# Performance work log

Hardware: AMD Instinct MI355X
Metric: run time of the kernel (lower is better)

## Reference

```python
import jax, jax.numpy as jnp
import numpy as np

NEG_SLOPE = 0.01  # torch F.leaky_relu default
BN_EPS = 1e-5
N_GRAPHS = 256


def _bn(x, gamma, beta):
    # training-mode BatchNorm1d per head over the node axis; x: [N, H, O]
    mu = x.mean(axis=0)
    var = x.var(axis=0)
    return (x - mu) * jax.lax.rsqrt(var + BN_EPS) * gamma + beta


def _gat_layer(h, src, dst, snorm, fcW, aS, aD, gamma, beta):
    # h: [N, Din]; fcW: [H, Din, O]; aS/aD/gamma/beta: [H, O]
    N = h.shape[0]
    z = jnp.einsum('nd,hdo->nho', h, fcW)                 # [N, H, O]
    el = jnp.einsum('nho,ho->nh', z, aS)                  # attn_fc src half
    er = jnp.einsum('nho,ho->nh', z, aD)                  # attn_fc dst half
    e = jax.nn.leaky_relu(el[src] + er[dst], NEG_SLOPE)   # [E, H]
    emax = jax.ops.segment_max(e, dst, num_segments=N)    # softmax over in-edges
    ee = jnp.exp(e - emax[dst])
    denom = jax.ops.segment_sum(ee, dst, num_segments=N)
    alpha = ee / denom[dst]                               # [E, H]
    msg = alpha[:, :, None] * z[src]                      # [E, H, O]
    agg = jax.ops.segment_sum(msg, dst, num_segments=N)   # [N, H, O]
    agg = agg * snorm[:, None, None]                      # graph_norm
    agg = _bn(agg, gamma, beta)                           # batch_norm
    out = jax.nn.elu(agg).reshape(N, -1)                  # concat heads
    return h + out                                        # residual (Din == H*O)


def setup_inputs() -> dict:
    key = jax.random.key(0)
    ks = jax.random.split(key, 32)
    N, E, G = 50000, 1600000, N_GRAPHS
    DIN, H, O, D, NC = 128, 8, 16, 128, 10
    L_mid = 3  # L-1 multi-head layers

    graph_ids = jnp.sort(jax.random.randint(ks[0], (N,), 0, G))
    counts = jax.ops.segment_sum(jnp.ones((N,), jnp.float32), graph_ids, num_segments=G)
    snorm = (1.0 / jnp.sqrt(jnp.maximum(counts, 1.0)))[graph_ids]  # nodes_num_norm_sqrt
    src = jax.random.randint(ks[1], (E,), 0, N)
    dst = jax.random.randint(ks[2], (E,), 0, N)

    def nrm(k, shape, s=0.1):
        return jax.random.normal(k, shape, jnp.float32) * s

    return {
        'nodes_feat': jax.random.normal(ks[3], (N, DIN), jnp.float32),
        'snorm': snorm,
        'emb_W': nrm(ks[4], (DIN, D)), 'emb_b': jnp.zeros((D,), jnp.float32),
        'fcW': nrm(ks[5], (L_mid, H, D, O)),
        'aS': nrm(ks[6], (L_mid, H, O)), 'aD': nrm(ks[7], (L_mid, H, O)),
        'gamma': jnp.ones((L_mid, H, O), jnp.float32),
        'beta': jnp.zeros((L_mid, H, O), jnp.float32),
        'fcW_last': nrm(ks[8], (1, D, D)),
        'aS_last': nrm(ks[9], (1, D)), 'aD_last': nrm(ks[10], (1, D)),
        'g_last': jnp.ones((1, D), jnp.float32), 'b_last': jnp.zeros((1, D), jnp.float32),
        'w1': nrm(ks[11], (D, D // 2)), 'b1': jnp.zeros((D // 2,), jnp.float32),
        'w2': nrm(ks[12], (D // 2, D // 4)), 'b2': jnp.zeros((D // 4,), jnp.float32),
        'w3': nrm(ks[13], (D // 4, NC)), 'b3': jnp.zeros((NC,), jnp.float32),
        'src': src, 'dst': dst, 'graph_ids': graph_ids,
    }


def reference(nodes_feat, snorm, emb_W, emb_b, fcW, aS, aD, gamma, beta,
              fcW_last, aS_last, aD_last, g_last, b_last,
              w1, b1, w2, b2, w3, b3, src, dst, graph_ids):
    h = nodes_feat @ emb_W + emb_b                        # embedding_h
    for l in range(fcW.shape[0]):                         # L-1 multi-head GAT layers
        h = _gat_layer(h, src, dst, snorm, fcW[l], aS[l], aD[l], gamma[l], beta[l])
    h = _gat_layer(h, src, dst, snorm, fcW_last, aS_last, aD_last, g_last, b_last)
    # mean_nodes readout over variable-size graphs
    counts = jax.ops.segment_sum(jnp.ones_like(snorm), graph_ids, num_segments=N_GRAPHS)
    hg = jax.ops.segment_sum(h, graph_ids, num_segments=N_GRAPHS)
    hg = hg / jnp.maximum(counts, 1.0)[:, None]           # [G, D]
    # MLPReadout: D -> D/2 -> D/4 -> n_classes
    y = jax.nn.relu(hg @ w1 + b1)
    y = jax.nn.relu(y @ w2 + b2)
    return y @ w3 + b3
```

## Files before the change

### kernel.cpp

```cpp
#include <hip/hip_runtime.h>
#include <hip/hip_bf16.h>
#include <hip/hip_fp16.h>

typedef __hip_bfloat16 bf16;
typedef __attribute__((ext_vector_type(8))) short short8;
typedef __attribute__((ext_vector_type(4))) float floatx4;

__device__ __forceinline__ float ldc(const void* p, size_t i, int code) {
    if (code == 1) return __bfloat162float(((const bf16*)p)[i]);
    if (code == 2) return __half2float(((const __half*)p)[i]);
    return ((const float*)p)[i];
}
__device__ __forceinline__ void stc(void* p, size_t i, int code, float v) {
    if (code == 1) ((bf16*)p)[i] = __float2bfloat16(v);
    else if (code == 2) ((__half*)p)[i] = __float2half(v);
    else ((float*)p)[i] = v;
}
__device__ __forceinline__ unsigned int pk2(float a, float b) {
    unsigned int ua = __float_as_uint(a); ua += 0x7fffu + ((ua >> 16) & 1u);
    unsigned int ub = __float_as_uint(b); ub += 0x7fffu + ((ub >> 16) & 1u);
    return (ua >> 16) | (ub & 0xffff0000u);
}

__global__ void k_detect(const unsigned short* __restrict__ g, int* __restrict__ code) {
    unsigned short a = g[0], b = g[1], c = g[2], d = g[3];
    int r;
    if (a == 0x3F80 && b == 0x3F80 && c == 0x3F80 && d == 0x3F80) r = 1;
    else if (a == 0x3C00 && b == 0x3C00 && c == 0x3C00 && d == 0x3C00) r = 2;
    else r = 3;
    *code = r;
}

__global__ void k_zero_i(int* p, int n) { int i = blockIdx.x * 256 + threadIdx.x; if (i < n) p[i] = 0; }
__global__ void k_zero_f(float* p, int n) { int i = blockIdx.x * 256 + threadIdx.x; if (i < n) p[i] = 0.f; }
__global__ void k_cvt(float* __restrict__ dst, const void* __restrict__ src, int n,
                      const int* __restrict__ codep) {
    int code = *codep;
    int i = blockIdx.x * 256 + threadIdx.x;
    if (i < n) dst[i] = ldc(src, i, code);
}
__global__ void k_sent(void* o, int n, float v, const int* codep) {
    int code = *codep;
    int i = blockIdx.x * 256 + threadIdx.x;
    if (i < n) stc(o, i, code, v);
}

struct CvtArgs { const void* src[16]; int off[17]; };
__global__ void k_cvt_all(float* __restrict__ dst, CvtArgs a,
                          const int* __restrict__ codep, int total) {
    int i = blockIdx.x * 256 + threadIdx.x;
    if (i >= total) return;
    int code = *codep;
    int seg = 0;
    #pragma unroll
    for (int k = 0; k < 15; ++k) seg += (i >= a.off[k + 1]) ? 1 : 0;
    dst[i] = ldc(a.src[seg], i - a.off[seg], code);
}

#define ETILE 8192
__global__ __launch_bounds__(256) void k_bcount(const int* __restrict__ dst,
        int* __restrict__ bcnt, int E, int nbuck) {
    __shared__ int h[200];
    int t = threadIdx.x;
    for (int i = t; i < nbuck; i += 256) h[i] = 0;
    __syncthreads();
    int e0 = blockIdx.x * ETILE;
    int n = min(ETILE, E - e0);
    for (int i = t; i < n; i += 256) atomicAdd(&h[dst[e0 + i] >> 8], 1);
    __syncthreads();
    for (int i = t; i < nbuck; i += 256)
        if (h[i]) atomicAdd(&bcnt[i], h[i]);
}

__global__ void k_scan(const int* __restrict__ cnt, int* __restrict__ off,
                       int* __restrict__ cur, int n) {
    __shared__ int sums[1024];
    int tid = threadIdx.x;
    int C = (n + 1023) >> 10;
    int lo = tid * C, hi = min(lo + C, n);
    int s = 0;
    for (int i = lo; i < hi; ++i) s += cnt[i];
    sums[tid] = s;
    __syncthreads();
    for (int o = 1; o < 1024; o <<= 1) {
        int v = (tid >= o) ? sums[tid - o] : 0;
        __syncthreads();
        sums[tid] += v;
        __syncthreads();
    }
    int run = (tid > 0) ? sums[tid - 1] : 0;
    for (int i = lo; i < hi; ++i) { off[i] = run; cur[i] = run; run += cnt[i]; }
    if (tid == 1023) off[n] = sums[1023];
}

__global__ __launch_bounds__(256) void k_bscat(const int* __restrict__ src,
        const int* __restrict__ dst, int* __restrict__ bcur,
        unsigned int* __restrict__ ebuf, int E, int nbuck) {
    __shared__ unsigned int eord[ETILE];
    __shared__ int cnt[200], lst[200], cur[200], gb[200];
    int t = threadIdx.x;
    int e0 = blockIdx.x * ETILE;
    int n = min(ETILE, E - e0);
    for (int i = t; i < nbuck; i += 256) cnt[i] = 0;
    __syncthreads();
    for (int i = t; i < n; i += 256) atomicAdd(&cnt[dst[e0 + i] >> 8], 1);
    __syncthreads();
    if (t == 0) {
        int run = 0;
        for (int b = 0; b < nbuck; ++b) { int c = cnt[b]; lst[b] = run; cur[b] = run; run += c; }
    }
    __syncthreads();
    for (int b = t; b < nbuck; b += 256)
        gb[b] = cnt[b] ? atomicAdd(&bcur[b], cnt[b]) : 0;
    for (int i = t; i < n; i += 256) {
        int d = dst[e0 + i];
        int pos = atomicAdd(&cur[d >> 8], 1);
        eord[pos] = ((unsigned int)d << 16) | (unsigned int)src[e0 + i];
    }
    __syncthreads();
    for (int i = t; i < n; i += 256) {
        unsigned int pk = eord[i];
        int b = pk >> 24;
        ebuf[gb[b] + (i - lst[b])] = pk;
    }
}

__global__ __launch_bounds__(256) void k_fscatter(const unsigned int* __restrict__ ebuf,
        const int* __restrict__ boff, int* __restrict__ row_off,
        unsigned short* __restrict__ col_src, int N, int E) {
    __shared__ int cnt[256], cur[256];
    int b = blockIdx.x, t = threadIdx.x;
    int lo = boff[b], hi = boff[b + 1];
    int nodelo = b << 8;
    cnt[t] = 0;
    __syncthreads();
    for (int j = lo + t; j < hi; j += 256)
        atomicAdd(&cnt[(int)(ebuf[j] >> 16) - nodelo], 1);
    __syncthreads();
    if (t == 0) {
        int run = lo;
        for (int i = 0; i < 256; ++i) { int c = cnt[i]; cur[i] = run; cnt[i] = run; run += c; }
    }
    __syncthreads();
    int node = nodelo + t;
    if (node < N) row_off[node] = cnt[t];
    if (t == 0 && b == (int)gridDim.x - 1) row_off[N] = E;
    for (int j = lo + t; j < hi; j += 256) {
        unsigned int pk = ebuf[j];
        int pos = atomicAdd(&cur[(int)(pk >> 16) - nodelo], 1);
        col_src[pos] = (unsigned short)(pk & 0xffffu);
    }
}

#define WB_STRIDE 136
#define WB_MAT 19584
__global__ void k_wtrans(const void* __restrict__ fcW, const void* __restrict__ fcW_last,
                         const void* __restrict__ emb_W,
                         const float* __restrict__ aSf, const float* __restrict__ aDf,
                         const float* __restrict__ aSlf, const float* __restrict__ aDlf,
                         unsigned short* __restrict__ Wb, const int* __restrict__ codep) {
    int code = *codep;
    int idx = blockIdx.x * 256 + threadIdx.x;
    if (idx >= 5 * WB_MAT) return;
    int m = idx / WB_MAT, rem = idx % WB_MAT;
    int c = rem / WB_STRIDE, k = rem % WB_STRIDE;
    float v = 0.f;
    if (k < 128) {
        if (m == 0) {
            if (c < 128) v = ldc(emb_W, k * 128 + c, code);
        } else if (m <= 3) {
            int l = m - 1;
            if (c < 128) v = ldc(fcW, l * 16384 + (c >> 4) * 2048 + k * 16 + (c & 15), code);
            else if (c < 136) {
                int hh = c - 128; float s = 0.f;
                for (int o = 0; o < 16; ++o)
                    s += ldc(fcW, l * 16384 + hh * 2048 + k * 16 + o, code) * aSf[l * 128 + hh * 16 + o];
                v = s;
            } else {
                int hh = c - 136; float s = 0.f;
                for (int o = 0; o < 16; ++o)
                    s += ldc(fcW, l * 16384 + hh * 2048 + k * 16 + o, code) * aDf[l * 128 + hh * 16 + o];
                v = s;
            }
        } else {
            if (c < 128) v = ldc(fcW_last, k * 128 + c, code);
            else if (c == 128) { float s = 0.f; for (int o = 0; o < 128; ++o) s += ldc(fcW_last, k * 128 + o, code) * aSlf[o]; v = s; }
            else if (c == 129) { float s = 0.f; for (int o = 0; o < 128; ++o) s += ldc(fcW_last, k * 128 + o, code) * aDlf[o]; v = s; }
        }
    }
    Wb[idx] = (unsigned short)(pk2(v, 0.f) & 0xffffu);
}

__global__ __launch_bounds__(256) void k_gemm(const void* __restrict__ Av, int a_raw,
        const int* __restrict__ codep, const unsigned short* __restrict__ Wbm,
        const float* __restrict__ bias, float* __restrict__ outf,
        unsigned int* __restrict__ zb,
        float* __restrict__ el, float* __restrict__ er, int H, int N) {
    __shared__ unsigned short Wl[WB_MAT];
    int tid = threadIdx.x;
    {
        const uint4* s4 = (const uint4*)Wbm;
        uint4* d4 = (uint4*)Wl;
        for (int i = tid; i < WB_MAT / 8; i += 256) d4[i] = s4[i];
    }
    int wave = tid >> 6, lane = tid & 63;
    int c15 = lane & 15, quad = lane >> 4;
    int rowb = blockIdx.x * 64 + wave * 16;
    int myrow = rowb + c15;
    bool rowok = myrow < N;
    int code = a_raw ? *codep : 3;

    floatx4 acc[9];
    #pragma unroll
    for (int i = 0; i < 9; ++i) acc[i] = (floatx4){0.f, 0.f, 0.f, 0.f};

    __syncthreads();
    #pragma unroll
    for (int ks = 0; ks < 4; ++ks) {
        int k0 = ks * 32 + quad * 8;
        short8 a;
        if (!rowok) {
            a = (short8){0, 0, 0, 0, 0, 0, 0, 0};
        } else if (code == 1) {
            union { uint4 u; short8 s; } cv;
            cv.u = *(const uint4*)((const unsigned short*)Av + (size_t)myrow * 128 + k0);
            a = cv.s;
        } else if (code == 3) {
            const float* ap = (const float*)Av + (size_t)myrow * 128 + k0;
            float4 x = *(const float4*)ap;
            float4 y = *(const float4*)(ap + 4);
            union { uint4 u; short8 s; } cv;
            cv.u = make_uint4(pk2(x.x, x.y), pk2(x.z, x.w), pk2(y.x, y.y), pk2(y.z, y.w));
            a = cv.s;
        } else {
            const __half* ap = (const __half*)Av + (size_t)myrow * 128 + k0;
            union { uint4 u; short8 s; } cv;
            cv.u = make_uint4(pk2(__half2float(ap[0]), __half2float(ap[1])),
                              pk2(__half2float(ap[2]), __half2float(ap[3])),
                              pk2(__half2float(ap[4]), __half2float(ap[5])),
                              pk2(__half2float(ap[6]), __half2float(ap[7])));
            a = cv.s;
        }
        #pragma unroll
        for (int ct = 0; ct < 9; ++ct) {
            union { uint4 u; short8 s; } bv;
            bv.u = *(const uint4*)&Wl[(ct * 16 + c15) * WB_STRIDE + k0];
            acc[ct] = __builtin_amdgcn_mfma_f32_16x16x32_bf16(a, bv.s, acc[ct], 0, 0, 0);
        }
    }

    if (zb == nullptr) {
        #pragma unroll
        for (int ct = 0; ct < 8; ++ct) {
            int c = ct * 16 + c15;
            float bj = bias ? bias[c] : 0.f;
            #pragma unroll
            for (int r = 0; r < 4; ++r) {
                int n = rowb + quad * 4 + r;
                if (n < N) outf[(size_t)n * 128 + c] = acc[ct][r] + bj;
            }
        }
    } else {
        #pragma unroll
        for (int ct = 0; ct < 8; ++ct) {
            #pragma unroll
            for (int r = 0; r < 4; ++r) {
                float v = acc[ct][r];
                float vx = __shfl_xor(v, 1);
                if ((c15 & 1) == 0) {
                    int n = rowb + quad * 4 + r;
                    if (n < N) zb[(size_t)n * 64 + ct * 8 + (c15 >> 1)] = pk2(v, vx);
                }
            }
        }
        #pragma unroll
        for (int r = 0; r < 4; ++r) {
            int n = rowb + quad * 4 + r;
            if (n < N) {
                float v = acc[8][r];
                if (c15 < H) el[n * H + c15] = v;
                else if (c15 < 2 * H) er[n * H + (c15 - H)] = v;
            }
        }
    }
}

__global__ __launch_bounds__(256) void k_agg(const unsigned int* __restrict__ zb,
        const float* __restrict__ el, const float* __restrict__ er,
        const int* __restrict__ row_off, const unsigned short* __restrict__ col_src,
        const float* __restrict__ snormf, float* __restrict__ agg,
        int N, int H, int hshift) {
    int n = blockIdx.x * 4 + (threadIdx.x >> 6);
    if (n >= N) return;
    int lane = threadIdx.x & 63;
    int hh = lane >> hshift;
    float ern = er[n * H + hh];
    int beg = row_off[n], end = row_off[n + 1];
    float l = 0.f, a0 = 0.f, a1 = 0.f;
    int j = beg;
    if (H == 8) {
        for (; j + 8 <= end; j += 8) {
            int sv = col_src[j + (lane & 7)];
            float e = el[sv * 8 + (lane >> 3)] + ern;
            e = (e > 0.f) ? e : 0.01f * e;
            float w = __expf(fminf(e, 60.f));
            #pragma unroll
            for (int i = 0; i < 8; ++i) {
                float wi = __shfl(w, i, 8);
                int si = col_src[j + i];
                unsigned int v = zb[(size_t)si * 64 + lane];
                l += wi;
                a0 = fmaf(wi, __uint_as_float(v << 16), a0);
                a1 = fmaf(wi, __uint_as_float(v & 0xffff0000u), a1);
            }
        }
    } else {
        for (; j + 16 <= end; j += 16) {
            int sv = col_src[j + (lane & 15)];
            float e = el[sv] + ern;
            e = (e > 0.f) ? e : 0.01f * e;
            float w = __expf(fminf(e, 60.f));
            #pragma unroll
            for (int i = 0; i < 16; ++i) {
                float wi = __shfl(w, i, 16);
                int si = col_src[j + i];
                unsigned int v = zb[(size_t)si * 64 + lane];
                l += wi;
                a0 = fmaf(wi, __uint_as_float(v << 16), a0);
                a1 = fmaf(wi, __uint_as_float(v & 0xffff0000u), a1);
            }
        }
    }
    for (; j < end; ++j) {
        int sa = col_src[j];
        float ea = el[sa * H + hh] + ern;
        unsigned int va = zb[(size_t)sa * 64 + lane];
        ea = (ea > 0.f) ? ea : 0.01f * ea;
        float wa = __expf(fminf(ea, 60.f));
        l += wa;
        a0 = fmaf(wa, __uint_as_float(va << 16), a0);
        a1 = fmaf(wa, __uint_as_float(va & 0xffff0000u), a1);
    }
    float sn = snormf[n];
    float inv = (end > beg) ? sn / l : 0.f;
    *(float2*)&agg[(size_t)n * 128 + 2 * lane] = make_float2(a0 * inv, a1 * inv);
}

#define BN_BLOCKS 256
__global__ void k_bnstats1(const float* __restrict__ agg, float* __restrict__ pstats, int N) {
    int c = threadIdx.x;
    float s = 0.f, q = 0.f;
    for (int n = blockIdx.x; n < N; n += gridDim.x) {
        float v = agg[(size_t)n * 128 + c];
        s += v; q += v * v;
    }
    pstats[blockIdx.x * 256 + c] = s;
    pstats[blockIdx.x * 256 + 128 + c] = q;
}
__global__ void k_bnstats2(const float* __restrict__ pstats, float* __restrict__ stats, int nb) {
    int c = threadIdx.x;
    float s0 = 0.f, s1 = 0.f, s2 = 0.f, s3 = 0.f;
    int b = 0;
    for (; b + 3 < nb; b += 4) {
        s0 += pstats[b * 256 + c];
        s1 += pstats[(b + 1) * 256 + c];
        s2 += pstats[(b + 2) * 256 + c];
        s3 += pstats[(b + 3) * 256 + c];
    }
    for (; b < nb; ++b) s0 += pstats[b * 256 + c];
    stats[c] = (s0 + s1) + (s2 + s3);
}
__global__ void k_bnapply(const float* __restrict__ agg, const float* __restrict__ stats,
        const float* __restrict__ gamma, const float* __restrict__ beta,
        float* __restrict__ h, int N) {
    int idx = blockIdx.x * 256 + threadIdx.x;
    if (idx >= N * 128) return;
    int c = idx & 127;
    float invN = 1.0f / (float)N;
    float mu = stats[c] * invN;
    float var = fmaxf(stats[128 + c] * invN - mu * mu, 0.f);
    float x = agg[idx];
    float xn = (x - mu) * rsqrtf(var + 1e-5f) * gamma[c] + beta[c];
    float y = (xn > 0.f) ? xn : (__expf(xn) - 1.0f);
    h[idx] += y;
}

__global__ void k_gsum(const float* __restrict__ h, const int* __restrict__ gids,
                       float* __restrict__ hg, float* __restrict__ gcnt, int N) {
    int c = threadIdx.x;
    int base = blockIdx.x * 64;
    int endi = min(base + 64, N);
    int gprev = -1; float acc = 0.f; int cnt = 0;
    for (int n = base; n < endi; ++n) {
        int g = gids[n];
        if (g != gprev) {
            if (gprev >= 0) {
                atomicAdd(&hg[gprev * 128 + c], acc);
                if (c == 0) atomicAdd(&gcnt[gprev], (float)cnt);
            }
            gprev = g; acc = 0.f; cnt = 0;
        }
        acc += h[(size_t)n * 128 + c];
        ++cnt;
    }
    if (gprev >= 0) {
        atomicAdd(&hg[gprev * 128 + c], acc);
        if (c == 0) atomicAdd(&gcnt[gprev], (float)cnt);
    }
}
__global__ void k_mlp(const float* __restrict__ hg, const float* __restrict__ gcnt,
        const float* __restrict__ w1, const float* __restrict__ b1,
        const float* __restrict__ w2, const float* __restrict__ b2,
        const float* __restrict__ w3, const float* __restrict__ b3,
        void* __restrict__ out, const int* __restrict__ codep) {
    __shared__ float xs[128], y1[64], y2[32];
    int g = blockIdx.x, tid = threadIdx.x;
    float inv = 1.0f / fmaxf(gcnt[g], 1.0f);
    xs[tid]      = hg[g * 128 + tid] * inv;
    xs[tid + 64] = hg[g * 128 + 64 + tid] * inv;
    __syncthreads();
    float a = b1[tid];
    for (int k = 0; k < 128; ++k) a = fmaf(xs[k], w1[k * 64 + tid], a);
    y1[tid] = fmaxf(a, 0.f);
    __syncthreads();
    if (tid < 32) {
        float a2 = b2[tid];
        for (int k = 0; k < 64; ++k) a2 = fmaf(y1[k], w2[k * 32 + tid], a2);
        y2[tid] = fmaxf(a2, 0.f);
    }
    __syncthreads();
    if (tid < 10) {
        float a3 = b3[tid];
        for (int k = 0; k < 32; ++k) a3 = fmaf(y2[k], w3[k * 10 + tid], a3);
        stc(out, g * 10 + tid, *codep, a3);
    }
}

extern "C" void kernel_launch(void* const* d_in, const int* in_sizes, int n_in,
                              void* d_out, int out_size, void* d_ws, size_t ws_size,
                              hipStream_t stream) {
    const void* nodes_feat = d_in[0];
    const void* snorm      = d_in[1];
    const void* emb_W      = d_in[2];
    const void* fcW        = d_in[4];
    const void* gamma      = d_in[7];
    const void* fcW_last   = d_in[9];
    const int*  src        = (const int*)d_in[20];
    const int*  dst        = (const int*)d_in[21];
    const int*  gids       = (const int*)d_in[22];

    const int N = 50000, E = 1600000, G = 256;
    const int NBUCK = (N + 255) >> 8;
    const int NTILE = (E + ETILE - 1) / ETILE;

    char* p = (char*)d_ws;
    auto alloc = [&](size_t bytes) { char* r = p; p += (bytes + 255) & ~(size_t)255; return r; };
    int*   code    = (int*)alloc(256);
    float* h       = (float*)alloc((size_t)N * 128 * 4);
    unsigned int* zb = (unsigned int*)alloc((size_t)N * 64 * 4);
    float* agg     = (float*)alloc((size_t)N * 128 * 4);
    float* el      = (float*)alloc((size_t)N * 8 * 4);
    float* er      = (float*)alloc((size_t)N * 8 * 4);
    int*   bcnt    = (int*)alloc((size_t)NBUCK * 4);
    int*   boff    = (int*)alloc((size_t)(NBUCK + 1) * 4);
    int*   bcur    = (int*)alloc((size_t)NBUCK * 4);
    unsigned int* ebuf = (unsigned int*)alloc((size_t)E * 4);
    int*   row_off = (int*)alloc((size_t)(N + 1) * 4);
    unsigned short* col_src = (unsigned short*)alloc((size_t)E * 2);
    unsigned short* Wb = (unsigned short*)alloc((size_t)5 * WB_MAT * 2);
    float* pstats  = (float*)alloc((size_t)BN_BLOCKS * 256 * 4);
    float* stats   = (float*)alloc(256 * 4);
    float* hg      = (float*)alloc((size_t)G * 128 * 4 + (size_t)G * 4);
    float* gcnt    = hg + (size_t)G * 128;
    float* snormf  = (float*)alloc((size_t)N * 4);
    float* params  = (float*)alloc(29226 * 4);

    const int OFF[17] = {0, 16384, 16512, 16896, 17280, 17664, 18048, 18176,
                         18304, 18432, 18560, 26752, 26816, 28864, 28896, 29216, 29226};
    float* emb_bf = params + OFF[1];
    float* aSf    = params + OFF[2];
    float* aDf    = params + OFF[3];
    float* gf     = params + OFF[4];
    float* bf     = params + OFF[5];
    float* aSlf   = params + OFF[6];
    float* aDlf   = params + OFF[7];
    float* glf    = params + OFF[8];
    float* blf    = params + OFF[9];
    float* w1f    = params + OFF[10];
    float* b1f    = params + OFF[11];
    float* w2f    = params + OFF[12];
    float* b2f_   = params + OFF[13];
    float* w3f    = params + OFF[14];
    float* b3f    = params + OFF[15];

    k_detect<<<1, 1, 0, stream>>>((const unsigned short*)gamma, code);

    bool ok = (n_in == 23) && (out_size == G * 10) &&
              (in_sizes[0] == N * 128) && (in_sizes[1] == N) &&
              (in_sizes[4] == 3 * 8 * 128 * 16) && (in_sizes[7] == 384) &&
              (in_sizes[9] == 16384) &&
              (in_sizes[20] == E) && (in_sizes[21] == E) && (in_sizes[22] == N);
    size_t need = (size_t)(p - (char*)d_ws);
    if (!ok || ws_size < need) {
        k_sent<<<(out_size + 255) / 256, 256, 0, stream>>>(d_out, out_size, ok ? 123.0f : 150.0f, code);
        return;
    }

    CvtArgs ca;
    const int srcidx[16] = {2, 3, 5, 6, 7, 8, 10, 11, 12, 13, 14, 15, 16, 17, 18, 19};
    for (int k = 0; k < 16; ++k) ca.src[k] = d_in[srcidx[k]];
    for (int k = 0; k < 17; ++k) ca.off[k] = OFF[k];
    k_cvt_all<<<(29226 + 255) / 256, 256, 0, stream>>>(params, ca, code, 29226);
    k_cvt<<<(N + 255) / 256, 256, 0, stream>>>(snormf, snorm, N, code);
    k_wtrans<<<(5 * WB_MAT + 255) / 256, 256, 0, stream>>>(
        fcW, fcW_last, emb_W, aSf, aDf, aSlf, aDlf, Wb, code);

    k_zero_i<<<1, 256, 0, stream>>>(bcnt, NBUCK);
    k_bcount<<<NTILE, 256, 0, stream>>>(dst, bcnt, E, NBUCK);
    k_scan<<<1, 1024, 0, stream>>>(bcnt, boff, bcur, NBUCK);
    k_bscat<<<NTILE, 256, 0, stream>>>(src, dst, bcur, ebuf, E, NBUCK);
    k_fscatter<<<NBUCK, 256, 0, stream>>>(ebuf, boff, row_off, col_src, N, E);

    int gblk = (N + 63) / 64;
    k_gemm<<<gblk, 256, 0, stream>>>(nodes_feat, 1, code, Wb, emb_bf, h,
                                     nullptr, nullptr, nullptr, 0, N);

    for (int l = 0; l < 4; ++l) {
        const unsigned short* Wl_ = Wb + (size_t)(l + 1) * WB_MAT;
        const float *gl, *bl; int H, hshift;
        if (l < 3) { gl = gf + l * 128; bl = bf + l * 128; H = 8; hshift = 3; }
        else       { gl = glf;          bl = blf;          H = 1; hshift = 6; }
        k_gemm<<<gblk, 256, 0, stream>>>(h, 0, code, Wl_, nullptr, nullptr,
                                         zb, el, er, H, N);
        k_agg<<<(N + 3) / 4, 256, 0, stream>>>(zb, el, er, row_off, col_src, snormf,
                                               agg, N, H, hshift);
        k_bnstats1<<<BN_BLOCKS, 128, 0, stream>>>(agg, pstats, N);
        k_bnstats2<<<1, 256, 0, stream>>>(pstats, stats, BN_BLOCKS);
        k_bnapply<<<(N * 128 + 255) / 256, 256, 0, stream>>>(agg, stats, gl, bl, h, N);
    }

    k_zero_f<<<(G * 129 + 255) / 256, 256, 0, stream>>>(hg, G * 129);
    k_gsum<<<(N + 63) / 64, 128, 0, stream>>>(h, gids, hg, gcnt, N);
    k_mlp<<<G, 64, 0, stream>>>(hg, gcnt, w1f, b1f, w2f, b2f_, w3f, b3f, d_out, code);
}
```

Before: 928.7 us.

## Split each node's edges across wave halves with 8-byte gathers in GAT aggregation

Measured after the change: 921.3 us. Within noise of the previous version (-0.8%).

```diff
diff --git a/kernel.cpp b/kernel.cpp
--- a/kernel.cpp
+++ b/kernel.cpp
@@ -33,19 +33,13 @@
 
 __global__ void k_zero_i(int* p, int n) { int i = blockIdx.x * 256 + threadIdx.x; if (i < n) p[i] = 0; }
 __global__ void k_zero_f(float* p, int n) { int i = blockIdx.x * 256 + threadIdx.x; if (i < n) p[i] = 0.f; }
-__global__ void k_cvt(float* __restrict__ dst, const void* __restrict__ src, int n,
-                      const int* __restrict__ codep) {
-    int code = *codep;
-    int i = blockIdx.x * 256 + threadIdx.x;
-    if (i < n) dst[i] = ldc(src, i, code);
-}
 __global__ void k_sent(void* o, int n, float v, const int* codep) {
     int code = *codep;
     int i = blockIdx.x * 256 + threadIdx.x;
     if (i < n) stc(o, i, code, v);
 }
 
-struct CvtArgs { const void* src[16]; int off[17]; };
+struct CvtArgs { const void* src[17]; int off[18]; };
 __global__ void k_cvt_all(float* __restrict__ dst, CvtArgs a,
                           const int* __restrict__ codep, int total) {
     int i = blockIdx.x * 256 + threadIdx.x;
@@ -53,7 +47,7 @@
     int code = *codep;
     int seg = 0;
     #pragma unroll
-    for (int k = 0; k < 15; ++k) seg += (i >= a.off[k + 1]) ? 1 : 0;
+    for (int k = 0; k < 16; ++k) seg += (i >= a.off[k + 1]) ? 1 : 0;
     dst[i] = ldc(a.src[seg], i - a.off[seg], code);
 }
 
@@ -289,61 +283,82 @@
         const float* __restrict__ el, const float* __restrict__ er,
         const int* __restrict__ row_off, const unsigned short* __restrict__ col_src,
         const float* __restrict__ snormf, float* __restrict__ agg,
-        int N, int H, int hshift) {
+        int N, int H) {
     int n = blockIdx.x * 4 + (threadIdx.x >> 6);
     if (n >= N) return;
     int lane = threadIdx.x & 63;
-    int hh = lane >> hshift;
-    float ern = er[n * H + hh];
+    int half = lane >> 5;
+    int sub = lane & 31;
+    int hha = (H == 8) ? (sub >> 2) : 0;
+    float er_t = er[n * H + hha];
+    float er_w = (H == 8) ? er[n * 8 + (lane >> 3)] : er_t;
     int beg = row_off[n], end = row_off[n + 1];
-    float l = 0.f, a0 = 0.f, a1 = 0.f;
+    float l = 0.f, c0 = 0.f, c1 = 0.f, c2 = 0.f, c3 = 0.f;
     int j = beg;
     if (H == 8) {
         for (; j + 8 <= end; j += 8) {
             int sv = col_src[j + (lane & 7)];
-            float e = el[sv * 8 + (lane >> 3)] + ern;
+            float e = el[sv * 8 + (lane >> 3)] + er_w;
             e = (e > 0.f) ? e : 0.01f * e;
             float w = __expf(fminf(e, 60.f));
             #pragma unroll
-            for (int i = 0; i < 8; ++i) {
-                float wi = __shfl(w, i, 8);
+            for (int p = 0; p < 4; ++p) {
+                int i = 2 * p + half;
+                float wi = __shfl(w, (hha << 3) + i);
                 int si = col_src[j + i];
-                unsigned int v = zb[(size_t)si * 64 + lane];
+                uint2 v = *(const uint2*)(zb + (size_t)si * 64 + sub * 2);
                 l += wi;
-                a0 = fmaf(wi, __uint_as_float(v << 16), a0);
-                a1 = fmaf(wi, __uint_as_float(v & 0xffff0000u), a1);
+                c0 = fmaf(wi, __uint_as_float(v.x << 16), c0);
+                c1 = fmaf(wi, __uint_as_float(v.x & 0xffff0000u), c1);
+                c2 = fmaf(wi, __uint_as_float(v.y << 16), c2);
+                c3 = fmaf(wi, __uint_as_float(v.y & 0xffff0000u), c3);
             }
         }
     } else {
         for (; j + 16 <= end; j += 16) {
             int sv = col_src[j + (lane & 15)];
-            float e = el[sv] + ern;
+            float e = el[sv] + er_w;
             e = (e > 0.f) ? e : 0.01f * e;
             float w = __expf(fminf(e, 60.f));
             #pragma unroll
-            for (int i = 0; i < 16; ++i) {
+            for (int p = 0; p < 8; ++p) {
+                int i = 2 * p + half;
                 float wi = __shfl(w, i, 16);
                 int si = col_src[j + i];
-                unsigned int v = zb[(size_t)si * 64 + lane];
+                uint2 v = *(const uint2*)(zb + (size_t)si * 64 + sub * 2);
                 l += wi;
-                a0 = fmaf(wi, __uint_as_float(v << 16), a0);
-                a1 = fmaf(wi, __uint_as_float(v & 0xffff0000u), a1);
-            }
-        }
-    }
-    for (; j < end; ++j) {
-        int sa = col_src[j];
-        float ea = el[sa * H + hh] + ern;
-        unsigned int va = zb[(size_t)sa * 64 + lane];
-        ea = (ea > 0.f) ? ea : 0.01f * ea;
-        float wa = __expf(fminf(ea, 60.f));
-        l += wa;
-        a0 = fmaf(wa, __uint_as_float(va << 16), a0);
-        a1 = fmaf(wa, __uint_as_float(va & 0xffff0000u), a1);
-    }
-    float sn = snormf[n];
-    float inv = (end > beg) ? sn / l : 0.f;
-    *(float2*)&agg[(size_t)n * 128 + 2 * lane] = make_float2(a0 * inv, a1 * inv);
+                c0 = fmaf(wi, __uint_as_float(v.x << 16), c0);
+                c1 = fmaf(wi, __uint_as_float(v.x & 0xffff0000u), c1);
+                c2 = fmaf(wi, __uint_as_float(v.y << 16), c2);
+                c3 = fmaf(wi, __uint_as_float(v.y & 0xffff0000u), c3);
+            }
+        }
+    }
+    for (; j < end; j += 2) {
+        int idx = j + half;
+        bool act = idx < end;
+        int si = col_src[act ? idx : j];
+        float e = el[si * H + hha] + er_t;
+        e = (e > 0.f) ? e : 0.01f * e;
+        float w = act ? __expf(fminf(e, 60.f)) : 0.f;
+        uint2 v = *(const uint2*)(zb + (size_t)si * 64 + sub * 2);
+        l += w;
+        c0 = fmaf(w, __uint_as_float(v.x << 16), c0);
+        c1 = fmaf(w, __uint_as_float(v.x & 0xffff0000u), c1);
+        c2 = fmaf(w, __uint_as_float(v.y << 16), c2);
+        c3 = fmaf(w, __uint_as_float(v.y & 0xffff0000u), c3);
+    }
+    l  += __shfl_xor(l, 32);
+    c0 += __shfl_xor(c0, 32);
+    c1 += __shfl_xor(c1, 32);
+    c2 += __shfl_xor(c2, 32);
+    c3 += __shfl_xor(c3, 32);
+    if (half == 0) {
+        float sn = snormf[n];
+        float inv = (end > beg) ? sn / l : 0.f;
+        float4 o = make_float4(c0 * inv, c1 * inv, c2 * inv, c3 * inv);
+        *(float4*)&agg[(size_t)n * 128 + 4 * sub] = o;
+    }
 }
 
 #define BN_BLOCKS 256
@@ -452,6 +467,7 @@
     const int N = 50000, E = 1600000, G = 256;
     const int NBUCK = (N + 255) >> 8;
     const int NTILE = (E + ETILE - 1) / ETILE;
+    const int PTOT = 29226 + N;
 
     char* p = (char*)d_ws;
     auto alloc = [&](size_t bytes) { char* r = p; p += (bytes + 255) & ~(size_t)255; return r; };
@@ -472,11 +488,10 @@
     float* stats   = (float*)alloc(256 * 4);
     float* hg      = (float*)alloc((size_t)G * 128 * 4 + (size_t)G * 4);
     float* gcnt    = hg + (size_t)G * 128;
-    float* snormf  = (float*)alloc((size_t)N * 4);
-    float* params  = (float*)alloc(29226 * 4);
-
-    const int OFF[17] = {0, 16384, 16512, 16896, 17280, 17664, 18048, 18176,
-                         18304, 18432, 18560, 26752, 26816, 28864, 28896, 29216, 29226};
+    float* params  = (float*)alloc((size_t)PTOT * 4);
+
+    const int OFF[18] = {0, 16384, 16512, 16896, 17280, 17664, 18048, 18176,
+                         18304, 18432, 18560, 26752, 26816, 28864, 28896, 29216, 29226, PTOT};
     float* emb_bf = params + OFF[1];
     float* aSf    = params + OFF[2];
     float* aDf    = params + OFF[3];
@@ -492,6 +507,7 @@
     float* b2f_   = params + OFF[13];
     float* w3f    = params + OFF[14];
     float* b3f    = params + OFF[15];
+    float* snormf = params + OFF[16];
 
     k_detect<<<1, 1, 0, stream>>>((const unsigned short*)gamma, code);
 
@@ -507,11 +523,10 @@
     }
 
     CvtArgs ca;
-    const int srcidx[16] = {2, 3, 5, 6, 7, 8, 10, 11, 12, 13, 14, 15, 16, 17, 18, 19};
-    for (int k = 0; k < 16; ++k) ca.src[k] = d_in[srcidx[k]];
-    for (int k = 0; k < 17; ++k) ca.off[k] = OFF[k];
-    k_cvt_all<<<(29226 + 255) / 256, 256, 0, stream>>>(params, ca, code, 29226);
-    k_cvt<<<(N + 255) / 256, 256, 0, stream>>>(snormf, snorm, N, code);
+    const int srcidx[17] = {2, 3, 5, 6, 7, 8, 10, 11, 12, 13, 14, 15, 16, 17, 18, 19, 1};
+    for (int k = 0; k < 17; ++k) ca.src[k] = d_in[srcidx[k]];
+    for (int k = 0; k < 18; ++k) ca.off[k] = OFF[k];
+    k_cvt_all<<<(PTOT + 255) / 256, 256, 0, stream>>>(params, ca, code, PTOT);
     k_wtrans<<<(5 * WB_MAT + 255) / 256, 256, 0, stream>>>(
         fcW, fcW_last, emb_W, aSf, aDf, aSlf, aDlf, Wb, code);
 
@@ -527,13 +542,13 @@
 
     for (int l = 0; l < 4; ++l) {
         const unsigned short* Wl_ = Wb + (size_t)(l + 1) * WB_MAT;
-        const float *gl, *bl; int H, hshift;
-        if (l < 3) { gl = gf + l * 128; bl = bf + l * 128; H = 8; hshift = 3; }
-        else       { gl = glf;          bl = blf;          H = 1; hshift = 6; }
+        const float *gl, *bl; int H;
+        if (l < 3) { gl = gf + l * 128; bl = bf + l * 128; H = 8; }
+        else       { gl = glf;          bl = blf;          H = 1; }
         k_gemm<<<gblk, 256, 0, stream>>>(h, 0, code, Wl_, nullptr, nullptr,
                                          zb, el, er, H, N);
         k_agg<<<(N + 3) / 4, 256, 0, stream>>>(zb, el, er, row_off, col_src, snormf,
-                                               agg, N, H, hshift);
+                                               agg, N, H);
         k_bnstats1<<<BN_BLOCKS, 128, 0, stream>>>(agg, pstats, N);
         k_bnstats2<<<1, 256, 0, stream>>>(pstats, stats, BN_BLOCKS);
         k_bnapply<<<(N * 128 + 255) / 256, 256, 0, stream>>>(agg, stats, gl, bl, h, N);
```
